# Kernel tuning notes

Hardware: AMD Instinct MI355X
Metric: run time of the kernel (lower is better)

Reference implementation:

```python
import jax, jax.numpy as jnp
import numpy as np

NEG = -1e20  # finite stand-in for -inf (exp underflows to 0; avoids nan grads)
S_RANGE = 19   # prune_range hard-coded in the module
TERM = 0       # termination/blank symbol
LM_ONLY = 0.25 # lm_only_scale; am_only_scale = 0 so that branch vanishes


def _mi(px, py):
    """RNN-T mutual-information forward DP (fast_rnnt mutual_information_recursion).
    px: (B,S,T+1) logprob of emitting symbol s+1 at (s,t); py: (B,S+1,T) blank logprobs.
    p[b,s,t] = logaddexp(p[b,s-1,t]+px[b,s-1,t], p[b,s,t-1]+py[b,s,t-1]); returns p[:,S,T]."""
    B, S, T1 = px.shape
    p0 = jnp.concatenate([jnp.zeros((B, 1), px.dtype),
                          jnp.cumsum(py[:, 0, :], axis=1)], axis=1)  # row s=0: (B,T+1)
    def outer(p_prev, inp):
        px_s, py_s = inp                 # (B,T+1), (B,T)
        b = p_prev + px_s                # vertical (emit) path into next row
        def inner(c, xs):
            b_t, py_t = xs
            c = jnp.logaddexp(b_t, c + py_t)
            return c, c
        _, rest = jax.lax.scan(inner, b[:, 0], (b[:, 1:].T, py_s.T))  # rest: (T,B)
        p_row = jnp.concatenate([b[:, :1], rest.T], axis=1)
        return p_row, None
    p_last, _ = jax.lax.scan(outer, p0,
                             (jnp.moveaxis(px, 1, 0), jnp.moveaxis(py[:, 1:, :], 1, 0)))
    return p_last[:, -1]  # (B,) total log-prob at (S,T)


def _smoothed_logprobs(am, lm, symbols):
    """fast_rnnt.get_rnnt_logprobs_smoothed with lm_only_scale=0.25, am_only_scale=0."""
    B, T, C = am.shape
    S = symbols.shape[1]
    lm_max = jnp.max(lm, axis=2, keepdims=True)   # (B,S+1,1)
    am_max = jnp.max(am, axis=2, keepdims=True)   # (B,T,1)
    lm_p = jnp.exp(lm - lm_max)
    am_p = jnp.exp(am - am_max)
    # normalizers[b,s,t] = log sum_k exp(lm[b,s,k] + am[b,t,k]) via matmul trick
    normalizers = jnp.log(jnp.einsum('bsc,btc->bst', lm_p, am_p)) \
        + lm_max + jnp.swapaxes(am_max, 1, 2)     # (B,S+1,T)
    sym_b = jnp.broadcast_to(symbols[:, None, :], (B, T, S))
    px_am = jnp.swapaxes(jnp.take_along_axis(am, sym_b, axis=2), 1, 2)  # (B,S,T)
    px_lm = jnp.take_along_axis(lm[:, :S], symbols[:, :, None], axis=2)  # (B,S,1)
    px = px_am + px_lm - normalizers[:, :S, :]
    lm_lsm = jax.nn.log_softmax(lm, axis=2)
    px_lmonly = jnp.take_along_axis(lm_lsm[:, :S], symbols[:, :, None], axis=2)
    comb = 1.0 - LM_ONLY
    px_i = comb * px + LM_ONLY * px_lmonly
    px_i = jnp.concatenate([px_i, jnp.full((B, S, 1), NEG, px_i.dtype)], axis=2)  # (B,S,T+1)
    py = am[:, :, TERM][:, None, :] + lm[:, :, TERM][:, :, None] - normalizers
    py_i = comb * py + LM_ONLY * lm_lsm[:, :, TERM][:, :, None]  # (B,S+1,T)
    return px_i, py_i


def _suffix_min(x):  # fast_rnnt _monotonic_lower_bound: x[t] = min(x[t:])
    return jax.lax.associative_scan(jnp.minimum, x, axis=1, reverse=True)


def _adjust_lower_bound(s_begin, r):  # fast_rnnt _adjust_pruning_lower_bound
    Tn = s_begin.shape[1]
    s_begin = _suffix_min(s_begin)
    off = (r - 1) * jnp.arange(Tn, dtype=s_begin.dtype)
    y = -(s_begin - off)
    y = jnp.maximum(_suffix_min(y), 0)
    return -(y - off)


def _prune_ranges(px_grad, py_grad, r):
    """fast_rnnt.get_rnnt_prune_ranges (all sequences full length)."""
    B, S, T1 = px_grad.shape
    T = T1 - 1
    py_pad = jnp.concatenate([py_grad, jnp.zeros((B, S + 1, 1), py_grad.dtype)], axis=2)
    tot = jnp.concatenate([px_grad, jnp.zeros((B, 1, T1), px_grad.dtype)], axis=1) + py_pad
    tot = jnp.concatenate([jnp.zeros((B, 1, T1), tot.dtype), tot], axis=1)  # (B,S+2,T1)
    cs = jnp.cumsum(tot, axis=1)
    diff = cs[:, r:, :] - cs[:, :-r, :]  # windowed occupancy sums
    s_begin = jnp.argmax(diff, axis=1)[:, :T].astype(jnp.int32)
    s_begin = _adjust_lower_bound(s_begin, r)
    return s_begin[:, :, None] + jnp.arange(r, dtype=jnp.int32)[None, None, :]  # (B,T,r)


def _pruned_logprobs(logits, symbols, ranges):
    """fast_rnnt.get_rnnt_logprobs_pruned."""
    B, T, r, C = logits.shape
    S = symbols.shape[1]
    norm = jax.nn.logsumexp(logits, axis=3)  # (B,T,r)
    sym_t = jnp.concatenate([symbols, jnp.full((B, 1), TERM, symbols.dtype)], axis=1)
    sym_b = jnp.broadcast_to(sym_t[:, None, :], (B, T, S + 1))
    pruned_sym = jnp.take_along_axis(sym_b, ranges, axis=2)  # (B,T,r)
    px = jnp.take_along_axis(logits, pruned_sym[..., None], axis=3)[..., 0] - norm
    py = logits[..., TERM] - norm
    def to_full(x):  # scatter (B,T,r) band into absolute symbol positions (B,T,S+1)
        pad = jnp.full((B, T, S + 1 - r), NEG, x.dtype)
        xf = jnp.concatenate([x, pad], axis=2)
        idx = (jnp.arange(S + 1)[None, None, :] - ranges[:, :, 0:1]) % (S + 1)
        return jnp.take_along_axis(xf, idx, axis=2)
    px_f = jnp.swapaxes(to_full(px), 1, 2)  # (B,S+1,T)
    py_f = jnp.swapaxes(to_full(py), 1, 2)  # (B,S+1,T)
    px_f = jnp.concatenate([px_f, jnp.full((B, S + 1, 1), NEG, px_f.dtype)], axis=2)[:, :S, :]
    return px_f, py_f  # (B,S,T+1), (B,S+1,T)


def _forward(am, lm, targets, joiner_w, joiner_b):
    px, py = _smoothed_logprobs(am, lm, targets)
    simple_loss = -jnp.mean(_mi(px, py))  # reduction='mean'
    # occupation-probability grads (values only, used for pruning)
    gpx, gpy = jax.grad(lambda a: jnp.sum(_mi(a[0], a[1])))(
        (jax.lax.stop_gradient(px), jax.lax.stop_gradient(py)))
    ranges = _prune_ranges(gpx, gpy, S_RANGE)  # (B,T,19) int32, constant wrt grads
    lm_pruned = jax.vmap(lambda l, rg: l[rg])(lm, ranges)  # (B,T,r,C) gather
    # joiner: logits = Linear(tanh(am_pruned + lm_pruned)); am broadcast over r
    logits = jnp.einsum('btrc,cd->btrd',
                        jnp.tanh(am[:, :, None, :] + lm_pruned), joiner_w) + joiner_b
    px2, py2 = _pruned_logprobs(logits.astype(jnp.float32), targets, ranges)
    pruned_loss = -jnp.mean(_mi(px2, py2))
    return 0.1 * simple_loss + pruned_loss


def setup_inputs() -> dict:
    key = jax.random.key(0)
    k = jax.random.split(key, 5)
    B, T, S, C = 8, 512, 128, 512
    return {
        "am": jax.random.normal(k[0], (B, T, C), jnp.float32),
        "lm": jax.random.normal(k[1], (B, S + 1, C), jnp.float32),
        "targets": jax.random.randint(k[2], (B, S), 1, C),  # blank=0 excluded
        "y_lens": jnp.full((B,), S, jnp.int32),             # full-length boundaries
        "joiner_w": 0.05 * jax.random.normal(k[3], (C, C), jnp.float32),
        "joiner_b": jnp.zeros((C,), jnp.float32),
    }


def reference(am, lm, targets, y_lens, joiner_w, joiner_b):
    # boundary = [0, 0, y_lens(=S), T] for every sequence
    return _forward(am, lm, targets, joiner_w, joiner_b)
```

## Files before the change

### kernel.cpp

```cpp
#include <hip/hip_runtime.h>
#include <math.h>

#define NEGV -1e20f
#define DPAD 132
#define RBOFF 16
#define ROWSA 676
#define RB(p,b) ((p) + ((size_t)(b) * ROWSA + RBOFF) * DPAD)
#define NROWS 77824

typedef __attribute__((ext_vector_type(4))) float floatx4;
typedef __attribute__((ext_vector_type(8))) short short8;


__device__ __forceinline__ float lae(float a, float b){
  float mx = fmaxf(a, b);
  float mn = fminf(a, b);
  return mx + __logf(1.f + __expf(mn - mx));
}

__device__ __forceinline__ short f2bf(float x){
  union { float f; unsigned u; } v; v.f = x;
  unsigned r = v.u + 0x7fffu + ((v.u >> 16) & 1u);
  return (short)(r >> 16);
}

__device__ __forceinline__ float tanh5(float x){
  float e = __expf(2.f * x);
  return 1.f - 2.f * __builtin_amdgcn_rcpf(e + 1.f);
}

__device__ __forceinline__ void gl_lds16(const short* __restrict__ g, short* l){
  __builtin_amdgcn_global_load_lds(
      (const __attribute__((address_space(1))) unsigned int*)g,
      (__attribute__((address_space(3))) unsigned int*)(unsigned long long)l,
      16, 0, 0);
}

__global__ __launch_bounds__(256) void k_row_stats(
    const float* __restrict__ in, float* __restrict__ outMax, float* __restrict__ outLse)
{
  int row = blockIdx.x;
  const float* r = in + (size_t)row * 512;
  int tid = threadIdx.x;
  float v0 = r[tid], v1 = r[tid + 256];
  float m = fmaxf(v0, v1);
  #pragma unroll
  for (int off = 32; off; off >>= 1) m = fmaxf(m, __shfl_xor(m, off, 64));
  __shared__ float sm[4];
  __shared__ float sbm;
  int wv = tid >> 6;
  if ((tid & 63) == 0) sm[wv] = m;
  __syncthreads();
  if (tid == 0) sbm = fmaxf(fmaxf(sm[0], sm[1]), fmaxf(sm[2], sm[3]));
  __syncthreads();
  float mx = sbm;
  if (tid == 0) outMax[row] = mx;
  if (outLse){
    float s = __expf(v0 - mx) + __expf(v1 - mx);
    #pragma unroll
    for (int off = 32; off; off >>= 1) s += __shfl_xor(s, off, 64);
    __shared__ float sp[4];
    if ((tid & 63) == 0) sp[wv] = s;
    __syncthreads();
    if (tid == 0) outLse[row] = mx + __logf(sp[0] + sp[1] + sp[2] + sp[3]);
  }
}

__global__ __launch_bounds__(256) void k_wb(const float* __restrict__ W, short* __restrict__ Wb){
  int idx = blockIdx.x * 256 + threadIdx.x;
  int d = idx >> 9, c = idx & 511;
  Wb[idx] = f2bf(W[c * 512 + d]);
}

__global__ __launch_bounds__(256) void k_norm(
    const float* __restrict__ am, const float* __restrict__ lm,
    const float* __restrict__ lmMax, const float* __restrict__ amMax,
    float* __restrict__ normv)
{
  int b = blockIdx.z;
  int s0 = blockIdx.y * 16;
  int t0 = blockIdx.x * 128;
  __shared__ float lmS[16][68];
  __shared__ float amS[128][68];
  int tid = threadIdx.x;
  int ts = tid >> 4, tt = tid & 15;
  float acc[8];
  #pragma unroll
  for (int j = 0; j < 8; ++j) acc[j] = 0.f;

  for (int k0 = 0; k0 < 512; k0 += 64){
    {
      int e = tid * 4;
      int rr = e >> 6, cc = e & 63;
      int s = s0 + rr;
      floatx4 o = {0.f, 0.f, 0.f, 0.f};
      if (s < 129){
        float mx = lmMax[b * 129 + s];
        floatx4 v = *(const floatx4*)(lm + ((size_t)(b * 129 + s)) * 512 + k0 + cc);
        o[0] = __expf(v[0] - mx); o[1] = __expf(v[1] - mx);
        o[2] = __expf(v[2] - mx); o[3] = __expf(v[3] - mx);
      }
      *(floatx4*)&lmS[rr][cc] = o;
    }
    #pragma unroll
    for (int i = 0; i < 8; ++i){
      int e = (tid + i * 256) * 4;
      int rr = e >> 6, cc = e & 63;
      float mx = amMax[b * 512 + t0 + rr];
      floatx4 v = *(const floatx4*)(am + ((size_t)(b * 512 + t0 + rr)) * 512 + k0 + cc);
      floatx4 o;
      o[0] = __expf(v[0] - mx); o[1] = __expf(v[1] - mx);
      o[2] = __expf(v[2] - mx); o[3] = __expf(v[3] - mx);
      *(floatx4*)&amS[rr][cc] = o;
    }
    __syncthreads();
    #pragma unroll 4
    for (int k = 0; k < 64; ++k){
      float a = lmS[ts][k];
      #pragma unroll
      for (int j = 0; j < 8; ++j) acc[j] += a * amS[tt + 16 * j][k];
    }
    __syncthreads();
  }
  int s = s0 + ts;
  if (s < 129){
    float lmx = lmMax[b * 129 + s];
    #pragma unroll
    for (int j = 0; j < 8; ++j){
      int t = t0 + tt + 16 * j;
      normv[((size_t)(b * 129 + s)) * 512 + t] = __logf(acc[j]) + lmx + amMax[b * 512 + t];
    }
  }
}

__global__ __launch_bounds__(256) void k_pxpy(
    const float* __restrict__ am, const float* __restrict__ lm,
    const int* __restrict__ targets, const float* __restrict__ normv,
    const float* __restrict__ lmLse, float* __restrict__ pxd, float* __restrict__ pyd)
{
  int bs = blockIdx.x;
  int b = bs / 129, s = bs % 129;
  float lm0 = lm[(size_t)bs * 512];
  float lse = lmLse[bs];
  int sym = 0; float lms = 0.f;
  if (s < 128){ sym = targets[b * 128 + s]; lms = lm[(size_t)bs * 512 + sym]; }
  const float* nrm = normv + (size_t)bs * 512;
  float* pydb = RB(pyd, b);
  float* pxdb = RB(pxd, b);
  for (int t = threadIdx.x; t < 513; t += 256){
    if (t < 512){
      float n = nrm[t];
      float a0 = am[((size_t)(b * 512 + t)) * 512];
      pydb[(size_t)(s + t) * DPAD + s] = 0.75f * (a0 + lm0 - n) + 0.25f * (lm0 - lse);
      if (s < 128){
        float as = am[((size_t)(b * 512 + t)) * 512 + sym];
        pxdb[(size_t)(s + t) * DPAD + s] = 0.75f * (as + lms - n) + 0.25f * (lms - lse);
      }
    } else if (s < 128){
      pxdb[(size_t)(s + 512) * DPAD + s] = NEGV;
    }
  }
}


__device__ __forceinline__ void dp_fwd_run(
    const float* __restrict__ pxb, const float* __restrict__ pyb,
    float* __restrict__ pab, float* __restrict__ tot, int b)
{
  int l = threadIdx.x;
  const int a = 2 * l;
  float curA = NEGV, curB = NEGV, curC = NEGV, send = NEGV;
  int paddr = (l - 1) << 2;

  float2 cpx = *(const float2*)(pxb - DPAD + a);
  float2 cpy = *(const float2*)(pyb - DPAD + a);
  float  cpz = pyb[-DPAD + 128];

  float2 b0px[8], b0py[8], b1px[8], b1py[8];
  float  b0pz[8], b1pz[8];
  float  outx[8], outy[8], outc[8];

  #pragma unroll
  for (int j = 0; j < 8; ++j){
    b0px[j] = *(const float2*)(pxb + (size_t)j * DPAD + a);
    b0py[j] = *(const float2*)(pyb + (size_t)j * DPAD + a);
    b0pz[j] = pyb[(size_t)j * DPAD + 128];
  }

  for (int i = 0; i < 40; ++i){
    int d0 = i * 16;
    #pragma unroll
    for (int j = 0; j < 8; ++j){
      b1px[j] = *(const float2*)(pxb + (size_t)(d0 + 8 + j) * DPAD + a);
      b1py[j] = *(const float2*)(pyb + (size_t)(d0 + 8 + j) * DPAD + a);
      b1pz[j] = pyb[(size_t)(d0 + 8 + j) * DPAD + 128];
    }
    __builtin_amdgcn_sched_barrier(0);
    #pragma unroll
    for (int j = 0; j < 8; ++j){
      int d = d0 + j;
      float2 pxm = j ? b0px[j - 1] : cpx;
      float2 pym = j ? b0py[j - 1] : cpy;
      float  pzm = j ? b0pz[j - 1] : cpz;
      float recv = __int_as_float(
          __builtin_amdgcn_ds_bpermute(paddr, __float_as_int(send)));
      int tA = d - a, tC = d - 128;
      float aaA = (l > 0) ? recv : NEGV;
      float bbA = (tA >= 1) ? curA + pym.x : NEGV;
      float nvA = lae(aaA, bbA);
      if (l == 0 && d == 0) nvA = 0.f;
      float aaB = curA + pxm.x;
      float bbB = (tA >= 2) ? curB + pym.y : NEGV;
      float nvB = lae(aaB, bbB);
      float aaC = curB + pxm.y;
      float bbC = (tC >= 1) ? curC + pzm : NEGV;
      float nvC = lae(aaC, bbC);
      if (tA >= 0 && tA <= 512) curA = nvA;
      if (tA >= 1 && tA <= 513) curB = nvB;
      if (tC >= 0 && tC <= 512) curC = nvC;
      send = curB + b0px[j].y;
      outx[j] = curA; outy[j] = curB; outc[j] = curC;
    }
    cpx = b0px[7]; cpy = b0py[7]; cpz = b0pz[7];
    if (pab){
      #pragma unroll
      for (int j = 0; j < 8; ++j)
        *(float2*)(pab + (size_t)(d0 + j) * DPAD + a) = make_float2(outx[j], outy[j]);
      if (l == 63){
        #pragma unroll
        for (int j = 0; j < 8; ++j)
          pab[(size_t)(d0 + j) * DPAD + 128] = outc[j];
      }
    }
    #pragma unroll
    for (int j = 0; j < 8; ++j){
      b0px[j] = *(const float2*)(pxb + (size_t)(d0 + 16 + j) * DPAD + a);
      b0py[j] = *(const float2*)(pyb + (size_t)(d0 + 16 + j) * DPAD + a);
      b0pz[j] = pyb[(size_t)(d0 + 16 + j) * DPAD + 128];
    }
    __builtin_amdgcn_sched_barrier(0);
    #pragma unroll
    for (int j = 0; j < 8; ++j){
      int d = d0 + 8 + j;
      float2 pxm = j ? b1px[j - 1] : cpx;
      float2 pym = j ? b1py[j - 1] : cpy;
      float  pzm = j ? b1pz[j - 1] : cpz;
      float recv = __int_as_float(
          __builtin_amdgcn_ds_bpermute(paddr, __float_as_int(send)));
      int tA = d - a, tC = d - 128;
      float aaA = (l > 0) ? recv : NEGV;
      float bbA = (tA >= 1) ? curA + pym.x : NEGV;
      float nvA = lae(aaA, bbA);
      float aaB = curA + pxm.x;
      float bbB = (tA >= 2) ? curB + pym.y : NEGV;
      float nvB = lae(aaB, bbB);
      float aaC = curB + pxm.y;
      float bbC = (tC >= 1) ? curC + pzm : NEGV;
      float nvC = lae(aaC, bbC);
      if (tA >= 0 && tA <= 512) curA = nvA;
      if (tA >= 1 && tA <= 513) curB = nvB;
      if (tC >= 0 && tC <= 512) curC = nvC;
      send = curB + b1px[j].y;
      outx[j] = curA; outy[j] = curB; outc[j] = curC;
    }
    cpx = b1px[7]; cpy = b1py[7]; cpz = b1pz[7];
    if (pab){
      #pragma unroll
      for (int j = 0; j < 8; ++j)
        *(float2*)(pab + (size_t)(d0 + 8 + j) * DPAD + a) = make_float2(outx[j], outy[j]);
      if (l == 63){
        #pragma unroll
        for (int j = 0; j < 8; ++j)
          pab[(size_t)(d0 + 8 + j) * DPAD + 128] = outc[j];
      }
    }
  }
  {
    float aaC = curB + cpx.y;
    float bbC = curC + cpz;
    curC = lae(aaC, bbC);
    if (l == 63){
      if (pab) pab[(size_t)640 * DPAD + 128] = curC;
      tot[b] = curC;
    }
  }
}

__device__ __forceinline__ void dp_bwd_run(
    const float* __restrict__ pxb, const float* __restrict__ pyb,
    float* __restrict__ beb)
{
  int l = threadIdx.x;
  const int a = 2 * l;
  float curA = NEGV, curB = NEGV, curC = NEGV, send = NEGV;
  int paddr = (l + 1) << 2;

  float2 b0px[8], b0py[8], b1px[8], b1py[8];
  float  b0pz[8], b1pz[8];
  float  outx[8], outy[8], outc[8];

  #pragma unroll
  for (int j = 0; j < 8; ++j){
    b0px[j] = *(const float2*)(pxb + (size_t)(640 - j) * DPAD + a);
    b0py[j] = *(const float2*)(pyb + (size_t)(640 - j) * DPAD + a);
    b0pz[j] = pyb[(size_t)(640 - j) * DPAD + 128];
  }

  for (int i = 0; i < 40; ++i){
    int d0 = 640 - 16 * i;
    #pragma unroll
    for (int j = 0; j < 8; ++j){
      b1px[j] = *(const float2*)(pxb + (size_t)(d0 - 8 - j) * DPAD + a);
      b1py[j] = *(const float2*)(pyb + (size_t)(d0 - 8 - j) * DPAD + a);
      b1pz[j] = pyb[(size_t)(d0 - 8 - j) * DPAD + 128];
    }
    __builtin_amdgcn_sched_barrier(0);
    #pragma unroll
    for (int j = 0; j < 8; ++j){
      int d = d0 - j;
      float2 pxA = b0px[j]; float2 pyA = b0py[j]; float pzA = b0pz[j];
      float recv = __int_as_float(
          __builtin_amdgcn_ds_bpermute(paddr, __float_as_int(send)));
      int tA = d - a, tB = tA - 1, tC = d - 128;
      float aaA = pxA.x + curB;
      float bbA = (tA <= 511) ? pyA.x + curA : NEGV;
      float nvA = lae(aaA, bbA);
      float up = (l < 63) ? recv : curC;
      float aaB = pxA.y + up;
      float bbB = (tB <= 511) ? pyA.y + curB : NEGV;
      float nvB = lae(aaB, bbB);
      float nvC = (tC <= 511) ? pzA + curC : NEGV;
      if (tC == 512) nvC = 0.f;
      if (tA >= 0 && tA <= 512) curA = nvA;
      if (tB >= 0 && tB <= 512) curB = nvB;
      if (tC >= 0 && tC <= 512) curC = nvC;
      send = curA;
      outx[j] = curA; outy[j] = curB; outc[j] = curC;
    }
    #pragma unroll
    for (int j = 0; j < 8; ++j)
      *(float2*)(beb + (size_t)(d0 - j) * DPAD + a) = make_float2(outx[j], outy[j]);
    if (l == 63){
      #pragma unroll
      for (int j = 0; j < 8; ++j)
        beb[(size_t)(d0 - j) * DPAD + 128] = outc[j];
    }
    #pragma unroll
    for (int j = 0; j < 8; ++j){
      b0px[j] = *(const float2*)(pxb + (size_t)(d0 - 16 - j) * DPAD + a);
      b0py[j] = *(const float2*)(pyb + (size_t)(d0 - 16 - j) * DPAD + a);
      b0pz[j] = pyb[(size_t)(d0 - 16 - j) * DPAD + 128];
    }
    __builtin_amdgcn_sched_barrier(0);
    #pragma unroll
    for (int j = 0; j < 8; ++j){
      int d = d0 - 8 - j;
      float2 pxA = b1px[j]; float2 pyA = b1py[j]; float pzA = b1pz[j];
      float recv = __int_as_float(
          __builtin_amdgcn_ds_bpermute(paddr, __float_as_int(send)));
      int tA = d - a, tB = tA - 1, tC = d - 128;
      float aaA = pxA.x + curB;
      float bbA = (tA <= 511) ? pyA.x + curA : NEGV;
      float nvA = lae(aaA, bbA);
      float up = (l < 63) ? recv : curC;
      float aaB = pxA.y + up;
      float bbB = (tB <= 511) ? pyA.y + curB : NEGV;
      float nvB = lae(aaB, bbB);
      float nvC = (tC <= 511) ? pzA + curC : NEGV;
      if (tC == 512) nvC = 0.f;
      if (tA >= 0 && tA <= 512) curA = nvA;
      if (tB >= 0 && tB <= 512) curB = nvB;
      if (tC >= 0 && tC <= 512) curC = nvC;
      send = curA;
      outx[j] = curA; outy[j] = curB; outc[j] = curC;
    }
    #pragma unroll
    for (int j = 0; j < 8; ++j)
      *(float2*)(beb + (size_t)(d0 - 8 - j) * DPAD + a) = make_float2(outx[j], outy[j]);
    if (l == 63){
      #pragma unroll
      for (int j = 0; j < 8; ++j)
        beb[(size_t)(d0 - 8 - j) * DPAD + 128] = outc[j];
    }
  }
  {
    float2 pxA = b0px[0]; float2 pyA = b0py[0];
    float recv = __int_as_float(
        __builtin_amdgcn_ds_bpermute(paddr, __float_as_int(send)));
    int tA = -a, tB = tA - 1;
    float aaA = pxA.x + curB;
    float bbA = (tA <= 511) ? pyA.x + curA : NEGV;
    float nvA = lae(aaA, bbA);
    float up = (l < 63) ? recv : curC;
    float aaB = pxA.y + up;
    float bbB = (tB <= 511) ? pyA.y + curB : NEGV;
    float nvB = lae(aaB, bbB);
    if (tA >= 0 && tA <= 512) curA = nvA;
    if (tB >= 0 && tB <= 512) curB = nvB;
    *(float2*)(beb + a) = make_float2(curA, curB);
    if (l == 63) beb[128] = curC;
  }
}

__global__ __launch_bounds__(64, 1) void k_dp_fb(
    const float* __restrict__ pxd, const float* __restrict__ pyd,
    float* __restrict__ pad, float* __restrict__ betad, float* __restrict__ tots)
{
  int blk = blockIdx.x;
  if (blk < 8){
    int b = blk;
    dp_fwd_run(RB(pxd, b), RB(pyd, b), RB(pad, b), tots, b);
  } else {
    int b = blk - 8;
    dp_bwd_run(RB(pxd, b), RB(pyd, b), RB(betad, b));
  }
}

__global__ __launch_bounds__(64, 1) void k_dp_f2(
    const float* __restrict__ pxd, const float* __restrict__ pyd,
    float* __restrict__ totp)
{
  int b = blockIdx.x;
  dp_fwd_run(RB(pxd, b), RB(pyd, b), (float*)nullptr, totp, b);
}

__global__ __launch_bounds__(256) void k_window(
    const float* __restrict__ pxd, const float* __restrict__ pyd,
    const float* __restrict__ pad, const float* __restrict__ betad,
    const float* __restrict__ tots, int* __restrict__ sbr)
{
  __shared__ float tote[129][66];
  int b = blockIdx.x >> 3;
  int t0 = (blockIdx.x & 7) << 6;
  const float* px = RB(pxd, b);
  const float* py = RB(pyd, b);
  const float* pa = RB(pad, b);
  const float* be = RB(betad, b);
  float tv = tots[b];
  int tid = threadIdx.x;
  int wv = tid >> 6, ln = tid & 63;
  for (int dd = wv; dd < 192; dd += 4){
    int d = t0 + dd;
    int slo = dd - 63 > 0 ? dd - 63 : 0;
    int shi = dd < 128 ? dd : 128;
    int s = slo + ln;
    if (s <= shi){
      size_t r0 = (size_t)d * DPAD + s, r1 = (size_t)(d + 1) * DPAD + s;
      float pav = pa[r0];
      float v = __expf(pav + py[r0] + be[r1] - tv);
      if (s < 128) v += __expf(pav + px[r0] + be[r1 + 1] - tv);
      tote[s][dd - s] = v;
    }
  }
  __syncthreads();
  if (tid < 64){
    int c = tid;
    float win = 0.f;
    for (int s = 0; s < 19; ++s) win += tote[s][c];
    float best = win; int arg = 0;
    for (int w2 = 1; w2 <= 110; ++w2){
      win += tote[w2 + 18][c] - tote[w2 - 1][c];
      if (win > best){ best = win; arg = w2; }
    }
    sbr[b * 512 + t0 + c] = arg;
  }
}

__global__ void k_adjust(const int* __restrict__ sbr, int* __restrict__ sbeg){
  if (threadIdx.x != 0) return;
  int b = blockIdx.x;
  const int* in = sbr + b * 512;
  int* out = sbeg + b * 512;
  int sbm = 1 << 30, ym = 1 << 30;
  for (int t = 511; t >= 0; --t){
    sbm = min(sbm, in[t]);
    int y = 18 * t - sbm;
    ym = min(ym, y);
    int yc = ym > 0 ? ym : 0;
    out[t] = 18 * t - yc;
  }
}

__global__ __launch_bounds__(256) void k_stageH(
    const float* __restrict__ am, const float* __restrict__ lm,
    const int* __restrict__ sbeg, short* __restrict__ Hb)
{
  __shared__ int rowAm[64], rowLm[64];
  int tid = threadIdx.x;
  int r0 = blockIdx.x * 64;
  if (tid < 64){
    int row = r0 + tid;
    int g = row / 19;
    int j = row - g * 19;
    int b = g >> 9, t = g & 511;
    int sidx = sbeg[b * 512 + t] + j;
    rowAm[tid] = (b * 512 + t) * 512;
    rowLm[tid] = (b * 129 + sidx) * 512;
  }
  __syncthreads();
  int row = tid >> 2;
  int kb = (tid & 3) * 8;
  const float* ap = am + (size_t)rowAm[row];
  const float* lp = lm + (size_t)rowLm[row];
  short* hp = Hb + (size_t)(r0 + row) * 512;
  #pragma unroll 4
  for (int i = 0; i < 16; ++i){
    int k = kb + i * 32;
    floatx4 a0 = *(const floatx4*)(ap + k);
    floatx4 a1 = *(const floatx4*)(ap + k + 4);
    floatx4 l0 = *(const floatx4*)(lp + k);
    floatx4 l1 = *(const floatx4*)(lp + k + 4);
    short8 h;
    h[0] = f2bf(tanh5(a0[0] + l0[0]));
    h[1] = f2bf(tanh5(a0[1] + l0[1]));
    h[2] = f2bf(tanh5(a0[2] + l0[2]));
    h[3] = f2bf(tanh5(a0[3] + l0[3]));
    h[4] = f2bf(tanh5(a1[0] + l1[0]));
    h[5] = f2bf(tanh5(a1[1] + l1[1]));
    h[6] = f2bf(tanh5(a1[2] + l1[2]));
    h[7] = f2bf(tanh5(a1[3] + l1[3]));
    *(short8*)(hp + k) = h;
  }
}

__global__ __launch_bounds__(256) void k_jgemm(
    const short* __restrict__ Hb, const short* __restrict__ Wb,
    const float* __restrict__ bias, const int* __restrict__ targets,
    const int* __restrict__ sbeg,
    float2* __restrict__ pms, float* __restrict__ pxraw, float* __restrict__ pyraw)
{
  __shared__ short As[128 * 32];
  __shared__ short Bs[128 * 32];
  __shared__ int rowSym[128];
  __shared__ float redM[128][2];
  __shared__ float redS[128][2];
  __shared__ float rowM[128];

  int tid = threadIdx.x;
  int bid = blockIdx.x;
  int xcd = bid & 7, idx = bid >> 3;
  int nb = idx & 3;
  int rt = xcd * 76 + (idx >> 2);
  int r0 = rt * 128, c0 = nb * 128;

  if (tid < 128){
    int row = r0 + tid;
    int g = row / 19;
    int j = row - g * 19;
    int b = g >> 9, t = g & 511;
    int sidx = sbeg[b * 512 + t] + j;
    rowSym[tid] = (sidx < 128) ? targets[b * 128 + sidx] : 0;
  }

  int w = tid >> 6, lane = tid & 63, q = lane >> 4, ln = lane & 15;
  int mBase = (w & 1) * 64;
  int nBase = (w >> 1) * 64;

  int sg0 = (w * 2) * 64 + lane;
  int sRow0 = sg0 >> 2, sKp0 = (sg0 & 3) << 3;
  int sg1 = sg0 + 64;
  int sRow1 = sg1 >> 2, sKp1 = (sg1 & 3) << 3;
  const short* Ag = Hb + (size_t)r0 * 512;
  const short* Bg = Wb + (size_t)c0 * 512;
  short* AsB0 = As + (w * 2) * 512;
  short* AsB1 = As + (w * 2 + 1) * 512;
  short* BsB0 = Bs + (w * 2) * 512;
  short* BsB1 = Bs + (w * 2 + 1) * 512;

  floatx4 acc[4][4];
  #pragma unroll
  for (int mt = 0; mt < 4; ++mt)
    #pragma unroll
    for (int nt = 0; nt < 4; ++nt) acc[mt][nt] = (floatx4){0.f, 0.f, 0.f, 0.f};

  for (int k0 = 0; k0 < 512; k0 += 32){
    gl_lds16(Ag + (size_t)sRow0 * 512 + k0 + sKp0, AsB0);
    gl_lds16(Ag + (size_t)sRow1 * 512 + k0 + sKp1, AsB1);
    gl_lds16(Bg + (size_t)sRow0 * 512 + k0 + sKp0, BsB0);
    gl_lds16(Bg + (size_t)sRow1 * 512 + k0 + sKp1, BsB1);
    __syncthreads();
    short8 af[4], bf[4];
    #pragma unroll
    for (int mt = 0; mt < 4; ++mt)
      af[mt] = *(const short8*)&As[(mBase + mt * 16 + ln) * 32 + q * 8];
    #pragma unroll
    for (int nt = 0; nt < 4; ++nt)
      bf[nt] = *(const short8*)&Bs[(nBase + nt * 16 + ln) * 32 + q * 8];
    __syncthreads();
    #pragma unroll
    for (int nt = 0; nt < 4; ++nt)
      #pragma unroll
      for (int mt = 0; mt < 4; ++mt)
        acc[mt][nt] = __builtin_amdgcn_mfma_f32_16x16x32_bf16(af[mt], bf[nt], acc[mt][nt], 0, 0, 0);
  }

  #pragma unroll
  for (int nt = 0; nt < 4; ++nt){
    int col = c0 + nBase + nt * 16 + ln;
    float bc = bias[col];
    #pragma unroll
    for (int mt = 0; mt < 4; ++mt)
      #pragma unroll
      for (int r = 0; r < 4; ++r){
        float v = acc[mt][nt][r] + bc;
        acc[mt][nt][r] = v;
        int rl = mBase + mt * 16 + q * 4 + r;
        if (col == 0) pyraw[r0 + rl] = v;
        if (col == rowSym[rl]) pxraw[r0 + rl] = v;
      }
  }
  #pragma unroll
  for (int mt = 0; mt < 4; ++mt)
    #pragma unroll
    for (int r = 0; r < 4; ++r){
      int rl = mBase + mt * 16 + q * 4 + r;
      float m = acc[mt][0][r];
      #pragma unroll
      for (int nt = 1; nt < 4; ++nt) m = fmaxf(m, acc[mt][nt][r]);
      m = fmaxf(m, __shfl_xor(m, 1, 16));
      m = fmaxf(m, __shfl_xor(m, 2, 16));
      m = fmaxf(m, __shfl_xor(m, 4, 16));
      m = fmaxf(m, __shfl_xor(m, 8, 16));
      if (ln == 0) redM[rl][w >> 1] = m;
    }
  __syncthreads();
  if (tid < 128) rowM[tid] = fmaxf(redM[tid][0], redM[tid][1]);
  __syncthreads();
  #pragma unroll
  for (int mt = 0; mt < 4; ++mt)
    #pragma unroll
    for (int r = 0; r < 4; ++r){
      int rl = mBase + mt * 16 + q * 4 + r;
      float rm = rowM[rl];
      float sa = 0.f;
      #pragma unroll
      for (int nt = 0; nt < 4; ++nt) sa += __expf(acc[mt][nt][r] - rm);
      sa += __shfl_xor(sa, 1, 16);
      sa += __shfl_xor(sa, 2, 16);
      sa += __shfl_xor(sa, 4, 16);
      sa += __shfl_xor(sa, 8, 16);
      if (ln == 0) redS[rl][w >> 1] = sa;
    }
  __syncthreads();
  if (tid < 128)
    pms[(size_t)nb * NROWS + r0 + tid] = make_float2(rowM[tid], redS[tid][0] + redS[tid][1]);
}

__global__ __launch_bounds__(256) void k_jfin(
    const float2* __restrict__ pms, const float* __restrict__ pxraw,
    const float* __restrict__ pyraw, float* __restrict__ pxv, float* __restrict__ pyv)
{
  int row = blockIdx.x * 256 + threadIdx.x;
  float2 p0 = pms[row];
  float2 p1 = pms[NROWS + row];
  float2 p2 = pms[2 * NROWS + row];
  float2 p3 = pms[3 * NROWS + row];
  float M = fmaxf(fmaxf(p0.x, p1.x), fmaxf(p2.x, p3.x));
  float S = p0.y * __expf(p0.x - M) + p1.y * __expf(p1.x - M)
          + p2.y * __expf(p2.x - M) + p3.y * __expf(p3.x - M);
  float norm = M + __logf(S);
  pxv[row] = pxraw[row] - norm;
  pyv[row] = pyraw[row] - norm;
}

__global__ __launch_bounds__(192) void k_band(
    const float* __restrict__ pxv, const float* __restrict__ pyv,
    const int* __restrict__ sbeg, float* __restrict__ px2d, float* __restrict__ py2d)
{
  int bd = blockIdx.x;
  int b = bd / 640, d = bd - b * 640;
  int s = threadIdx.x;
  int t = d - s;
  if (s > 128 || t < 0 || t > 512) return;
  size_t addr = ((size_t)b * ROWSA + RBOFF + d) * DPAD + s;
  if (s < 128){
    float v;
    if (t == 512) v = NEGV;
    else {
      int start = sbeg[b * 512 + t];
      int j = s - start;
      v = (j >= 0 && j < 19) ? pxv[((size_t)(b * 512 + t)) * 19 + j] : NEGV;
    }
    px2d[addr] = v;
  }
  if (t <= 511){
    int start = sbeg[b * 512 + t];
    int j = s - start;
    py2d[addr] = (j >= 0 && j < 19) ? pyv[((size_t)(b * 512 + t)) * 19 + j] : NEGV;
  }
}

__global__ void k_final(const float* __restrict__ tots, const float* __restrict__ totp,
                        float* __restrict__ out){
  if (blockIdx.x == 0 && threadIdx.x == 0){
    float a = 0.f, c = 0.f;
    for (int i = 0; i < 8; ++i){ a += tots[i]; c += totp[i]; }
    out[0] = -0.1f * (a * 0.125f) - (c * 0.125f);
  }
}

extern "C" void kernel_launch(void* const* d_in, const int* in_sizes, int n_in,
                              void* d_out, int out_size, void* d_ws, size_t ws_size,
                              hipStream_t stream){
  (void)in_sizes; (void)n_in; (void)out_size; (void)ws_size;
  const float* am      = (const float*)d_in[0];
  const float* lm      = (const float*)d_in[1];
  const int*   targets = (const int*)d_in[2];
  const float* W       = (const float*)d_in[4];
  const float* bias    = (const float*)d_in[5];
  float* out = (float*)d_out;

  char* base = (char*)d_ws;
  size_t off = 0;
  auto alloc = [&](size_t bytes) -> char* {
    char* r = base + off;
    off += (bytes + 255) & ~(size_t)255;
    return r;
  };
  const size_t DARR = 8ull * ROWSA * DPAD * 4;
  float* amMax = (float*)alloc(8ull * 512 * 4);
  float* lmMax = (float*)alloc(8ull * 129 * 4);
  float* lmLse = (float*)alloc(8ull * 129 * 4);
  float* normv = (float*)alloc(8ull * 129 * 512 * 4);
  float* pxd   = (float*)alloc(DARR);
  float* pyd   = (float*)alloc(DARR);
  float* pad   = (float*)alloc(DARR);
  float* betad = (float*)alloc(DARR);
  float* tots  = (float*)alloc(8 * 4);
  float* totp  = (float*)alloc(8 * 4);
  int*   sbr   = (int*)alloc(8ull * 512 * 4);
  int*   sbeg  = (int*)alloc(8ull * 512 * 4);
  float* pxv   = (float*)alloc((size_t)NROWS * 4);
  float* pyv   = (float*)alloc((size_t)NROWS * 4);
  short* Wb    = (short*)alloc((512ull * 512 + 512) * 2);
  short* Hb    = (short*)alloc(((size_t)NROWS * 512 + 512) * 2);
  float2* pms  = (float2*)alloc(4ull * NROWS * 8);
  float* pxraw = (float*)alloc((size_t)NROWS * 4);
  float* pyraw = (float*)alloc((size_t)NROWS * 4);
  float* px2d  = pxd;
  float* py2d  = pyd;

  k_row_stats<<<dim3(4096), dim3(256), 0, stream>>>(am, amMax, (float*)nullptr);
  k_row_stats<<<dim3(1032), dim3(256), 0, stream>>>(lm, lmMax, lmLse);
  k_wb<<<dim3(1024), dim3(256), 0, stream>>>(W, Wb);
  k_norm<<<dim3(4, 9, 8), dim3(256), 0, stream>>>(am, lm, lmMax, amMax, normv);
  k_pxpy<<<dim3(1032), dim3(256), 0, stream>>>(am, lm, targets, normv, lmLse, pxd, pyd);
  k_dp_fb<<<dim3(16), dim3(64), 0, stream>>>(pxd, pyd, pad, betad, tots);
  k_window<<<dim3(64), dim3(256), 0, stream>>>(pxd, pyd, pad, betad, tots, sbr);
  k_adjust<<<dim3(8), dim3(64), 0, stream>>>(sbr, sbeg);
  k_stageH<<<dim3(1216), dim3(256), 0, stream>>>(am, lm, sbeg, Hb);
  k_jgemm<<<dim3(2432), dim3(256), 0, stream>>>(Hb, Wb, bias, targets, sbeg, pms, pxraw, pyraw);
  k_jfin<<<dim3(304), dim3(256), 0, stream>>>(pms, pxraw, pyraw, pxv, pyv);
  k_band<<<dim3(5120), dim3(192), 0, stream>>>(pxv, pyv, sbeg, px2d, py2d);
  k_dp_f2<<<dim3(8), dim3(64), 0, stream>>>(px2d, py2d, totp);
  k_final<<<dim3(1), dim3(64), 0, stream>>>(tots, totp, out);
}
```

Measured before the change: 567.5 us.

## Interleave px/py into float2 diagonal layout with dwordx4 prefetch in DP kernels

```diff
diff --git a/kernel.cpp b/kernel.cpp
--- a/kernel.cpp
+++ b/kernel.cpp
@@ -7,6 +7,8 @@
 #define ROWSA 676
 #define RB(p,b) ((p) + ((size_t)(b) * ROWSA + RBOFF) * DPAD)
 #define NROWS 77824
+#define R2A 688
+#define R2OFF 16
 
 typedef __attribute__((ext_vector_type(4))) float floatx4;
 typedef __attribute__((ext_vector_type(8))) short short8;
@@ -34,6 +36,16 @@
       (const __attribute__((address_space(1))) unsigned int*)g,
       (__attribute__((address_space(3))) unsigned int*)(unsigned long long)l,
       16, 0, 0);
+}
+
+__device__ __forceinline__ floatx4 gld4(const float* p){
+  floatx4 r;
+  asm volatile("global_load_dwordx4 %0, %1, off" : "=v"(r) : "v"(p));
+  return r;
+}
+template<int N> __device__ __forceinline__ void waitv(){
+  asm volatile("s_waitcnt vmcnt(%0)" :: "i"(N));
+  __builtin_amdgcn_sched_barrier(0);
 }
 
 __global__ __launch_bounds__(256) void k_row_stats(
@@ -136,7 +148,7 @@
 __global__ __launch_bounds__(256) void k_pxpy(
     const float* __restrict__ am, const float* __restrict__ lm,
     const int* __restrict__ targets, const float* __restrict__ normv,
-    const float* __restrict__ lmLse, float* __restrict__ pxd, float* __restrict__ pyd)
+    const float* __restrict__ lmLse, float2* __restrict__ pxy, float* __restrict__ py128g)
 {
   int bs = blockIdx.x;
   int b = bs / 129, s = bs % 129;
@@ -145,296 +157,206 @@
   int sym = 0; float lms = 0.f;
   if (s < 128){ sym = targets[b * 128 + s]; lms = lm[(size_t)bs * 512 + sym]; }
   const float* nrm = normv + (size_t)bs * 512;
-  float* pydb = RB(pyd, b);
-  float* pxdb = RB(pxd, b);
+  float2* pxb = pxy + ((size_t)b * R2A + R2OFF) * 128;
   for (int t = threadIdx.x; t < 513; t += 256){
     if (t < 512){
       float n = nrm[t];
       float a0 = am[((size_t)(b * 512 + t)) * 512];
-      pydb[(size_t)(s + t) * DPAD + s] = 0.75f * (a0 + lm0 - n) + 0.25f * (lm0 - lse);
+      float pyv_ = 0.75f * (a0 + lm0 - n) + 0.25f * (lm0 - lse);
       if (s < 128){
         float as = am[((size_t)(b * 512 + t)) * 512 + sym];
-        pxdb[(size_t)(s + t) * DPAD + s] = 0.75f * (as + lms - n) + 0.25f * (lms - lse);
+        float pxv_ = 0.75f * (as + lms - n) + 0.25f * (lms - lse);
+        pxb[(size_t)(s + t) * 128 + s] = make_float2(pxv_, pyv_);
+      } else {
+        py128g[(size_t)b * R2A + R2OFF + 128 + t] = pyv_;
       }
     } else if (s < 128){
-      pxdb[(size_t)(s + 512) * DPAD + s] = NEGV;
-    }
-  }
-}
-
-
+      pxb[(size_t)(s + 512) * 128 + s] = make_float2(NEGV, NEGV);
+    }
+  }
+}
+
+
+#define FWDSTEP(vp, vc, pz, d)                                            \
+  {                                                                       \
+    float recv = __int_as_float(                                          \
+        __builtin_amdgcn_ds_bpermute(paddr, __float_as_int(send)));       \
+    int tA = (d) - a, tC = (d) - 128;                                     \
+    float aaA = (l > 0) ? recv : NEGV;                                    \
+    float bbA = (tA >= 1) ? curA + (vp)[1] : NEGV;                        \
+    float nvA = lae(aaA, bbA);                                            \
+    if (l == 0 && (d) == 0) nvA = 0.f;                                    \
+    float aaB = curA + (vp)[0];                                           \
+    float bbB = (tA >= 2) ? curB + (vp)[3] : NEGV;                        \
+    float nvB = lae(aaB, bbB);                                            \
+    float aaC = curB + (vp)[2];                                           \
+    float bbC = (tC >= 1) ? curC + (pz) : NEGV;                           \
+    float nvC = lae(aaC, bbC);                                            \
+    if (tA >= 0 && tA <= 512) curA = nvA;                                 \
+    if (tA >= 1 && tA <= 513) curB = nvB;                                 \
+    if (tC >= 0 && tC <= 512) curC = nvC;                                 \
+    send = curB + (vc)[2];                                                \
+    if (HasStore){                                                        \
+      *(float2*)(pab + (size_t)(d) * DPAD + a) = make_float2(curA, curB); \
+      if (l == 63) pab[(size_t)(d) * DPAD + 128] = curC;                  \
+    }                                                                     \
+  }
+
+template<bool HasStore>
 __device__ __forceinline__ void dp_fwd_run(
-    const float* __restrict__ pxb, const float* __restrict__ pyb,
+    const float2* __restrict__ pxy, const float* pzs,
     float* __restrict__ pab, float* __restrict__ tot, int b)
 {
   int l = threadIdx.x;
   const int a = 2 * l;
+  const char* Pb = (const char*)(pxy + ((size_t)b * R2A + R2OFF) * 128);
   float curA = NEGV, curB = NEGV, curC = NEGV, send = NEGV;
   int paddr = (l - 1) << 2;
 
-  float2 cpx = *(const float2*)(pxb - DPAD + a);
-  float2 cpy = *(const float2*)(pyb - DPAD + a);
-  float  cpz = pyb[-DPAD + 128];
-
-  float2 b0px[8], b0py[8], b1px[8], b1py[8];
-  float  b0pz[8], b1pz[8];
-  float  outx[8], outy[8], outc[8];
-
-  #pragma unroll
-  for (int j = 0; j < 8; ++j){
-    b0px[j] = *(const float2*)(pxb + (size_t)j * DPAD + a);
-    b0py[j] = *(const float2*)(pyb + (size_t)j * DPAD + a);
-    b0pz[j] = pyb[(size_t)j * DPAD + 128];
-  }
-
-  for (int i = 0; i < 40; ++i){
-    int d0 = i * 16;
-    #pragma unroll
-    for (int j = 0; j < 8; ++j){
-      b1px[j] = *(const float2*)(pxb + (size_t)(d0 + 8 + j) * DPAD + a);
-      b1py[j] = *(const float2*)(pyb + (size_t)(d0 + 8 + j) * DPAD + a);
-      b1pz[j] = pyb[(size_t)(d0 + 8 + j) * DPAD + 128];
-    }
+  floatx4 A[16], Bv[16];
+  floatx4 c4 = gld4((const float*)(Pb - 1024 + a * 8));
+  #pragma unroll
+  for (int j = 0; j < 16; ++j)
+    A[j] = gld4((const float*)(Pb + (ptrdiff_t)j * 1024 + a * 8));
+  waitv<0>();
+
+  for (int i = 0; i < 20; ++i){
+    int base = 32 * i;
     __builtin_amdgcn_sched_barrier(0);
     #pragma unroll
-    for (int j = 0; j < 8; ++j){
-      int d = d0 + j;
-      float2 pxm = j ? b0px[j - 1] : cpx;
-      float2 pym = j ? b0py[j - 1] : cpy;
-      float  pzm = j ? b0pz[j - 1] : cpz;
-      float recv = __int_as_float(
-          __builtin_amdgcn_ds_bpermute(paddr, __float_as_int(send)));
-      int tA = d - a, tC = d - 128;
-      float aaA = (l > 0) ? recv : NEGV;
-      float bbA = (tA >= 1) ? curA + pym.x : NEGV;
-      float nvA = lae(aaA, bbA);
-      if (l == 0 && d == 0) nvA = 0.f;
-      float aaB = curA + pxm.x;
-      float bbB = (tA >= 2) ? curB + pym.y : NEGV;
-      float nvB = lae(aaB, bbB);
-      float aaC = curB + pxm.y;
-      float bbC = (tC >= 1) ? curC + pzm : NEGV;
-      float nvC = lae(aaC, bbC);
-      if (tA >= 0 && tA <= 512) curA = nvA;
-      if (tA >= 1 && tA <= 513) curB = nvB;
-      if (tC >= 0 && tC <= 512) curC = nvC;
-      send = curB + b0px[j].y;
-      outx[j] = curA; outy[j] = curB; outc[j] = curC;
-    }
-    cpx = b0px[7]; cpy = b0py[7]; cpz = b0pz[7];
-    if (pab){
-      #pragma unroll
-      for (int j = 0; j < 8; ++j)
-        *(float2*)(pab + (size_t)(d0 + j) * DPAD + a) = make_float2(outx[j], outy[j]);
-      if (l == 63){
-        #pragma unroll
-        for (int j = 0; j < 8; ++j)
-          pab[(size_t)(d0 + j) * DPAD + 128] = outc[j];
-      }
-    }
-    #pragma unroll
-    for (int j = 0; j < 8; ++j){
-      b0px[j] = *(const float2*)(pxb + (size_t)(d0 + 16 + j) * DPAD + a);
-      b0py[j] = *(const float2*)(pyb + (size_t)(d0 + 16 + j) * DPAD + a);
-      b0pz[j] = pyb[(size_t)(d0 + 16 + j) * DPAD + 128];
-    }
+    for (int j = 0; j < 16; ++j)
+      Bv[j] = gld4((const float*)(Pb + (ptrdiff_t)(base + 16 + j) * 1024 + a * 8));
+    if (HasStore) waitv<48>(); else waitv<16>();
+    #pragma unroll
+    for (int j = 0; j < 16; ++j){
+      int d = base + j;
+      floatx4 vp = j ? A[j - 1] : c4;
+      FWDSTEP(vp, A[j], pzs[R2OFF + d - 1], d)
+    }
+    c4 = A[15];
     __builtin_amdgcn_sched_barrier(0);
     #pragma unroll
-    for (int j = 0; j < 8; ++j){
-      int d = d0 + 8 + j;
-      float2 pxm = j ? b1px[j - 1] : cpx;
-      float2 pym = j ? b1py[j - 1] : cpy;
-      float  pzm = j ? b1pz[j - 1] : cpz;
-      float recv = __int_as_float(
-          __builtin_amdgcn_ds_bpermute(paddr, __float_as_int(send)));
-      int tA = d - a, tC = d - 128;
-      float aaA = (l > 0) ? recv : NEGV;
-      float bbA = (tA >= 1) ? curA + pym.x : NEGV;
-      float nvA = lae(aaA, bbA);
-      float aaB = curA + pxm.x;
-      float bbB = (tA >= 2) ? curB + pym.y : NEGV;
-      float nvB = lae(aaB, bbB);
-      float aaC = curB + pxm.y;
-      float bbC = (tC >= 1) ? curC + pzm : NEGV;
-      float nvC = lae(aaC, bbC);
-      if (tA >= 0 && tA <= 512) curA = nvA;
-      if (tA >= 1 && tA <= 513) curB = nvB;
-      if (tC >= 0 && tC <= 512) curC = nvC;
-      send = curB + b1px[j].y;
-      outx[j] = curA; outy[j] = curB; outc[j] = curC;
-    }
-    cpx = b1px[7]; cpy = b1py[7]; cpz = b1pz[7];
-    if (pab){
-      #pragma unroll
-      for (int j = 0; j < 8; ++j)
-        *(float2*)(pab + (size_t)(d0 + 8 + j) * DPAD + a) = make_float2(outx[j], outy[j]);
-      if (l == 63){
-        #pragma unroll
-        for (int j = 0; j < 8; ++j)
-          pab[(size_t)(d0 + 8 + j) * DPAD + 128] = outc[j];
-      }
-    }
+    for (int j = 0; j < 16; ++j)
+      A[j] = gld4((const float*)(Pb + (ptrdiff_t)(base + 32 + j) * 1024 + a * 8));
+    if (HasStore) waitv<48>(); else waitv<16>();
+    #pragma unroll
+    for (int j = 0; j < 16; ++j){
+      int d = base + 16 + j;
+      floatx4 vp = j ? Bv[j - 1] : c4;
+      FWDSTEP(vp, Bv[j], pzs[R2OFF + d - 1], d)
+    }
+    c4 = Bv[15];
   }
   {
-    float aaC = curB + cpx.y;
-    float bbC = curC + cpz;
+    float aaC = curB + c4[2];
+    float bbC = curC + pzs[R2OFF + 639];
     curC = lae(aaC, bbC);
     if (l == 63){
-      if (pab) pab[(size_t)640 * DPAD + 128] = curC;
+      if (HasStore) pab[(size_t)640 * DPAD + 128] = curC;
       tot[b] = curC;
     }
   }
 }
 
+#define BWDSTEP(v, pz, d)                                                 \
+  {                                                                       \
+    float recv = __int_as_float(                                          \
+        __builtin_amdgcn_ds_bpermute(paddr, __float_as_int(send)));       \
+    int tA = (d) - a, tB = tA - 1, tC = (d) - 128;                        \
+    float aaA = (v)[0] + curB;                                            \
+    float bbA = (tA <= 511) ? (v)[1] + curA : NEGV;                       \
+    float nvA = lae(aaA, bbA);                                            \
+    float up = (l < 63) ? recv : curC;                                    \
+    float aaB = (v)[2] + up;                                              \
+    float bbB = (tB <= 511) ? (v)[3] + curB : NEGV;                       \
+    float nvB = lae(aaB, bbB);                                            \
+    float nvC = (tC <= 511) ? (pz) + curC : NEGV;                         \
+    if (tC == 512) nvC = 0.f;                                             \
+    if (tA >= 0 && tA <= 512) curA = nvA;                                 \
+    if (tB >= 0 && tB <= 512) curB = nvB;                                 \
+    if (tC >= 0 && tC <= 512) curC = nvC;                                 \
+    send = curA;                                                          \
+    *(float2*)(beb + (size_t)(d) * DPAD + a) = make_float2(curA, curB);   \
+    if (l == 63) beb[(size_t)(d) * DPAD + 128] = curC;                    \
+  }
+
 __device__ __forceinline__ void dp_bwd_run(
-    const float* __restrict__ pxb, const float* __restrict__ pyb,
-    float* __restrict__ beb)
+    const float2* __restrict__ pxy, const float* pzs,
+    float* __restrict__ beb, int b)
 {
   int l = threadIdx.x;
   const int a = 2 * l;
+  const char* Pb = (const char*)(pxy + ((size_t)b * R2A + R2OFF) * 128);
   float curA = NEGV, curB = NEGV, curC = NEGV, send = NEGV;
   int paddr = (l + 1) << 2;
 
-  float2 b0px[8], b0py[8], b1px[8], b1py[8];
-  float  b0pz[8], b1pz[8];
-  float  outx[8], outy[8], outc[8];
-
-  #pragma unroll
-  for (int j = 0; j < 8; ++j){
-    b0px[j] = *(const float2*)(pxb + (size_t)(640 - j) * DPAD + a);
-    b0py[j] = *(const float2*)(pyb + (size_t)(640 - j) * DPAD + a);
-    b0pz[j] = pyb[(size_t)(640 - j) * DPAD + 128];
-  }
-
-  for (int i = 0; i < 40; ++i){
-    int d0 = 640 - 16 * i;
-    #pragma unroll
-    for (int j = 0; j < 8; ++j){
-      b1px[j] = *(const float2*)(pxb + (size_t)(d0 - 8 - j) * DPAD + a);
-      b1py[j] = *(const float2*)(pyb + (size_t)(d0 - 8 - j) * DPAD + a);
-      b1pz[j] = pyb[(size_t)(d0 - 8 - j) * DPAD + 128];
-    }
+  floatx4 A[16], Bv[16];
+  #pragma unroll
+  for (int j = 0; j < 16; ++j)
+    A[j] = gld4((const float*)(Pb + (ptrdiff_t)(640 - j) * 1024 + a * 8));
+  waitv<0>();
+
+  for (int i = 0; i < 20; ++i){
+    int base = 640 - 32 * i;
     __builtin_amdgcn_sched_barrier(0);
     #pragma unroll
-    for (int j = 0; j < 8; ++j){
-      int d = d0 - j;
-      float2 pxA = b0px[j]; float2 pyA = b0py[j]; float pzA = b0pz[j];
-      float recv = __int_as_float(
-          __builtin_amdgcn_ds_bpermute(paddr, __float_as_int(send)));
-      int tA = d - a, tB = tA - 1, tC = d - 128;
-      float aaA = pxA.x + curB;
-      float bbA = (tA <= 511) ? pyA.x + curA : NEGV;
-      float nvA = lae(aaA, bbA);
-      float up = (l < 63) ? recv : curC;
-      float aaB = pxA.y + up;
-      float bbB = (tB <= 511) ? pyA.y + curB : NEGV;
-      float nvB = lae(aaB, bbB);
-      float nvC = (tC <= 511) ? pzA + curC : NEGV;
-      if (tC == 512) nvC = 0.f;
-      if (tA >= 0 && tA <= 512) curA = nvA;
-      if (tB >= 0 && tB <= 512) curB = nvB;
-      if (tC >= 0 && tC <= 512) curC = nvC;
-      send = curA;
-      outx[j] = curA; outy[j] = curB; outc[j] = curC;
-    }
-    #pragma unroll
-    for (int j = 0; j < 8; ++j)
-      *(float2*)(beb + (size_t)(d0 - j) * DPAD + a) = make_float2(outx[j], outy[j]);
-    if (l == 63){
-      #pragma unroll
-      for (int j = 0; j < 8; ++j)
-        beb[(size_t)(d0 - j) * DPAD + 128] = outc[j];
-    }
-    #pragma unroll
-    for (int j = 0; j < 8; ++j){
-      b0px[j] = *(const float2*)(pxb + (size_t)(d0 - 16 - j) * DPAD + a);
-      b0py[j] = *(const float2*)(pyb + (size_t)(d0 - 16 - j) * DPAD + a);
-      b0pz[j] = pyb[(size_t)(d0 - 16 - j) * DPAD + 128];
+    for (int j = 0; j < 16; ++j)
+      Bv[j] = gld4((const float*)(Pb + (ptrdiff_t)(base - 16 - j) * 1024 + a * 8));
+    waitv<48>();
+    #pragma unroll
+    for (int j = 0; j < 16; ++j){
+      int d = base - j;
+      BWDSTEP(A[j], pzs[R2OFF + d], d)
     }
     __builtin_amdgcn_sched_barrier(0);
     #pragma unroll
-    for (int j = 0; j < 8; ++j){
-      int d = d0 - 8 - j;
-      float2 pxA = b1px[j]; float2 pyA = b1py[j]; float pzA = b1pz[j];
-      float recv = __int_as_float(
-          __builtin_amdgcn_ds_bpermute(paddr, __float_as_int(send)));
-      int tA = d - a, tB = tA - 1, tC = d - 128;
-      float aaA = pxA.x + curB;
-      float bbA = (tA <= 511) ? pyA.x + curA : NEGV;
-      float nvA = lae(aaA, bbA);
-      float up = (l < 63) ? recv : curC;
-      float aaB = pxA.y + up;
-      float bbB = (tB <= 511) ? pyA.y + curB : NEGV;
-      float nvB = lae(aaB, bbB);
-      float nvC = (tC <= 511) ? pzA + curC : NEGV;
-      if (tC == 512) nvC = 0.f;
-      if (tA >= 0 && tA <= 512) curA = nvA;
-      if (tB >= 0 && tB <= 512) curB = nvB;
-      if (tC >= 0 && tC <= 512) curC = nvC;
-      send = curA;
-      outx[j] = curA; outy[j] = curB; outc[j] = curC;
-    }
-    #pragma unroll
-    for (int j = 0; j < 8; ++j)
-      *(float2*)(beb + (size_t)(d0 - 8 - j) * DPAD + a) = make_float2(outx[j], outy[j]);
-    if (l == 63){
-      #pragma unroll
-      for (int j = 0; j < 8; ++j)
-        beb[(size_t)(d0 - 8 - j) * DPAD + 128] = outc[j];
-    }
-  }
-  {
-    float2 pxA = b0px[0]; float2 pyA = b0py[0];
-    float recv = __int_as_float(
-        __builtin_amdgcn_ds_bpermute(paddr, __float_as_int(send)));
-    int tA = -a, tB = tA - 1;
-    float aaA = pxA.x + curB;
-    float bbA = (tA <= 511) ? pyA.x + curA : NEGV;
-    float nvA = lae(aaA, bbA);
-    float up = (l < 63) ? recv : curC;
-    float aaB = pxA.y + up;
-    float bbB = (tB <= 511) ? pyA.y + curB : NEGV;
-    float nvB = lae(aaB, bbB);
-    if (tA >= 0 && tA <= 512) curA = nvA;
-    if (tB >= 0 && tB <= 512) curB = nvB;
-    *(float2*)(beb + a) = make_float2(curA, curB);
-    if (l == 63) beb[128] = curC;
-  }
+    for (int j = 0; j < 16; ++j)
+      A[j] = gld4((const float*)(Pb + (ptrdiff_t)(base - 32 - j) * 1024 + a * 8));
+    waitv<48>();
+    #pragma unroll
+    for (int j = 0; j < 16; ++j){
+      int d = base - 16 - j;
+      BWDSTEP(Bv[j], pzs[R2OFF + d], d)
+    }
+  }
+  waitv<0>();
+  BWDSTEP(A[0], pzs[R2OFF], 0)
 }
 
 __global__ __launch_bounds__(64, 1) void k_dp_fb(
-    const float* __restrict__ pxd, const float* __restrict__ pyd,
-    float* __restrict__ pad, float* __restrict__ betad, float* __restrict__ tots)
-{
+    const float2* __restrict__ pxy, const float* __restrict__ py128g,
+    float* __restrict__ pad_, float* __restrict__ betad, float* __restrict__ tots)
+{
+  __shared__ float pzs[704];
   int blk = blockIdx.x;
-  if (blk < 8){
-    int b = blk;
-    dp_fwd_run(RB(pxd, b), RB(pyd, b), RB(pad, b), tots, b);
-  } else {
-    int b = blk - 8;
-    dp_bwd_run(RB(pxd, b), RB(pyd, b), RB(betad, b));
-  }
+  int l = threadIdx.x;
+  int b = blk & 7;
+  for (int k = l; k < R2A; k += 64) pzs[k] = py128g[(size_t)b * R2A + k];
+  if (blk < 8) dp_fwd_run<true>(pxy, pzs, RB(pad_, b), tots, b);
+  else         dp_bwd_run(pxy, pzs, RB(betad, b), b);
 }
 
 __global__ __launch_bounds__(64, 1) void k_dp_f2(
-    const float* __restrict__ pxd, const float* __restrict__ pyd,
+    const float2* __restrict__ pxy, const float* __restrict__ py128g2,
     float* __restrict__ totp)
 {
+  __shared__ float pzs[704];
   int b = blockIdx.x;
-  dp_fwd_run(RB(pxd, b), RB(pyd, b), (float*)nullptr, totp, b);
+  int l = threadIdx.x;
+  for (int k = l; k < R2A; k += 64) pzs[k] = py128g2[(size_t)b * R2A + k];
+  dp_fwd_run<false>(pxy, pzs, (float*)nullptr, totp, b);
 }
 
 __global__ __launch_bounds__(256) void k_window(
-    const float* __restrict__ pxd, const float* __restrict__ pyd,
-    const float* __restrict__ pad, const float* __restrict__ betad,
+    const float2* __restrict__ pxy, const float* __restrict__ py128g,
+    const float* __restrict__ pad_, const float* __restrict__ betad,
     const float* __restrict__ tots, int* __restrict__ sbr)
 {
   __shared__ float tote[129][66];
   int b = blockIdx.x >> 3;
   int t0 = (blockIdx.x & 7) << 6;
-  const float* px = RB(pxd, b);
-  const float* py = RB(pyd, b);
-  const float* pa = RB(pad, b);
+  const float2* pxyb = pxy + ((size_t)b * R2A + R2OFF) * 128;
+  const float* pa = RB(pad_, b);
   const float* be = RB(betad, b);
   float tv = tots[b];
   int tid = threadIdx.x;
@@ -447,8 +369,15 @@
     if (s <= shi){
       size_t r0 = (size_t)d * DPAD + s, r1 = (size_t)(d + 1) * DPAD + s;
       float pav = pa[r0];
-      float v = __expf(pav + py[r0] + be[r1] - tv);
-      if (s < 128) v += __expf(pav + px[r0] + be[r1 + 1] - tv);
+      float v;
+      if (s < 128){
+        float2 pp = pxyb[(size_t)d * 128 + s];
+        v = __expf(pav + pp.y + be[r1] - tv)
+          + __expf(pav + pp.x + be[r1 + 1] - tv);
+      } else {
+        float pyv_ = py128g[(size_t)b * R2A + R2OFF + d];
+        v = __expf(pav + pyv_ + be[r1] - tv);
+      }
       tote[s][dd - s] = v;
     }
   }
@@ -665,28 +594,29 @@
 
 __global__ __launch_bounds__(192) void k_band(
     const float* __restrict__ pxv, const float* __restrict__ pyv,
-    const int* __restrict__ sbeg, float* __restrict__ px2d, float* __restrict__ py2d)
+    const int* __restrict__ sbeg, float2* __restrict__ pxy2, float* __restrict__ py128g2)
 {
   int bd = blockIdx.x;
   int b = bd / 640, d = bd - b * 640;
   int s = threadIdx.x;
   int t = d - s;
   if (s > 128 || t < 0 || t > 512) return;
-  size_t addr = ((size_t)b * ROWSA + RBOFF + d) * DPAD + s;
   if (s < 128){
-    float v;
-    if (t == 512) v = NEGV;
+    float pxv_, pyv_;
+    if (t == 512){ pxv_ = NEGV; pyv_ = NEGV; }
     else {
       int start = sbeg[b * 512 + t];
       int j = s - start;
-      v = (j >= 0 && j < 19) ? pxv[((size_t)(b * 512 + t)) * 19 + j] : NEGV;
-    }
-    px2d[addr] = v;
-  }
-  if (t <= 511){
+      bool in = (j >= 0 && j < 19);
+      pxv_ = in ? pxv[((size_t)(b * 512 + t)) * 19 + j] : NEGV;
+      pyv_ = in ? pyv[((size_t)(b * 512 + t)) * 19 + j] : NEGV;
+    }
+    pxy2[((size_t)b * R2A + R2OFF + d) * 128 + s] = make_float2(pxv_, pyv_);
+  } else if (t <= 511){
     int start = sbeg[b * 512 + t];
-    int j = s - start;
-    py2d[addr] = (j >= 0 && j < 19) ? pyv[((size_t)(b * 512 + t)) * 19 + j] : NEGV;
+    int j = 128 - start;
+    py128g2[(size_t)b * R2A + R2OFF + d] =
+        (j >= 0 && j < 19) ? pyv[((size_t)(b * 512 + t)) * 19 + j] : NEGV;
   }
 }
 
@@ -722,9 +652,10 @@
   float* lmMax = (float*)alloc(8ull * 129 * 4);
   float* lmLse = (float*)alloc(8ull * 129 * 4);
   float* normv = (float*)alloc(8ull * 129 * 512 * 4);
-  float* pxd   = (float*)alloc(DARR);
-  float* pyd   = (float*)alloc(DARR);
-  float* pad   = (float*)alloc(DARR);
+  float2* pxyd = (float2*)alloc(8ull * R2A * 128 * 8);
+  float* py128g  = (float*)alloc(8ull * R2A * 4);
+  float* py128g2 = (float*)alloc(8ull * R2A * 4);
+  float* pad_  = (float*)alloc(DARR);
   float* betad = (float*)alloc(DARR);
   float* tots  = (float*)alloc(8 * 4);
   float* totp  = (float*)alloc(8 * 4);
@@ -737,21 +668,20 @@
   float2* pms  = (float2*)alloc(4ull * NROWS * 8);
   float* pxraw = (float*)alloc((size_t)NROWS * 4);
   float* pyraw = (float*)alloc((size_t)NROWS * 4);
-  float* px2d  = pxd;
-  float* py2d  = pyd;
+  float2* pxy2 = pxyd;
 
   k_row_stats<<<dim3(4096), dim3(256), 0, stream>>>(am, amMax, (float*)nullptr);
   k_row_stats<<<dim3(1032), dim3(256), 0, stream>>>(lm, lmMax, lmLse);
   k_wb<<<dim3(1024), dim3(256), 0, stream>>>(W, Wb);
   k_norm<<<dim3(4, 9, 8), dim3(256), 0, stream>>>(am, lm, lmMax, amMax, normv);
-  k_pxpy<<<dim3(1032), dim3(256), 0, stream>>>(am, lm, targets, normv, lmLse, pxd, pyd);
-  k_dp_fb<<<dim3(16), dim3(64), 0, stream>>>(pxd, pyd, pad, betad, tots);
-  k_window<<<dim3(64), dim3(256), 0, stream>>>(pxd, pyd, pad, betad, tots, sbr);
+  k_pxpy<<<dim3(1032), dim3(256), 0, stream>>>(am, lm, targets, normv, lmLse, pxyd, py128g);
+  k_dp_fb<<<dim3(16), dim3(64), 0, stream>>>(pxyd, py128g, pad_, betad, tots);
+  k_window<<<dim3(64), dim3(256), 0, stream>>>(pxyd, py128g, pad_, betad, tots, sbr);
   k_adjust<<<dim3(8), dim3(64), 0, stream>>>(sbr, sbeg);
   k_stageH<<<dim3(1216), dim3(256), 0, stream>>>(am, lm, sbeg, Hb);
   k_jgemm<<<dim3(2432), dim3(256), 0, stream>>>(Hb, Wb, bias, targets, sbeg, pms, pxraw, pyraw);
   k_jfin<<<dim3(304), dim3(256), 0, stream>>>(pms, pxraw, pyraw, pxv, pyv);
-  k_band<<<dim3(5120), dim3(192), 0, stream>>>(pxv, pyv, sbeg, px2d, py2d);
-  k_dp_f2<<<dim3(8), dim3(64), 0, stream>>>(px2d, py2d, totp);
+  k_band<<<dim3(5120), dim3(192), 0, stream>>>(pxv, pyv, sbeg, pxy2, py128g2);
+  k_dp_f2<<<dim3(8), dim3(64), 0, stream>>>(pxy2, py128g2, totp);
   k_final<<<dim3(1), dim3(64), 0, stream>>>(tots, totp, out);
 }
```

New measurement: 573.0 us. About the same (+1.0%).
